# Kernel optimization log

Measured on AMD Instinct MI355X. Metric: run time of the kernel, lower is better.

The kernel has to match this reference:

```python
import jax, jax.numpy as jnp
import numpy as np
from jax import lax

D_CONV = 4


def setup_inputs() -> dict:
    key = jax.random.key(0)
    ks = jax.random.split(key, 8)
    b, L, d_model = 2, 1024, 1024
    d_inner, d_state = 2048, 16
    s = 0.02  # weight scale
    return {
        "x": jax.random.normal(ks[0], (b, L, d_model), jnp.float32),
        "in_w": jax.random.normal(ks[1], (2 * d_inner, d_model), jnp.float32) * s,
        "in_b": jnp.zeros((2 * d_inner,), jnp.float32),
        "conv_w": jax.random.normal(ks[2], (d_inner, 1, D_CONV), jnp.float32) * s,
        "conv_b": jnp.zeros((d_inner,), jnp.float32),
        "xproj_w": jax.random.normal(ks[3], (2 * d_state + 1, d_inner), jnp.float32) * s,
        "dt_w": jax.random.normal(ks[4], (d_inner, 1), jnp.float32) * s,
        "dt_b": jnp.zeros((d_inner,), jnp.float32),
        "A_log": jax.random.normal(ks[5], (d_inner, d_state), jnp.float32),
        "D": jnp.ones((d_inner,), jnp.float32),
        "out_w": jax.random.normal(ks[6], (d_model, d_inner), jnp.float32) * s,
    }


def reference(x, in_w, in_b, conv_w, conv_b, xproj_w, dt_w, dt_b, A_log, D, out_w):
    b, L, _ = x.shape
    d_inner = conv_w.shape[0]
    d_state = A_log.shape[1]

    xz = x @ in_w.T + in_b                       # (b, L, 2*d_inner)
    xh, z = jnp.split(xz, 2, axis=-1)            # each (b, L, d_inner)

    # depthwise causal conv1d (torch pads d_conv-1 both sides then slices [:L])
    xc = jnp.transpose(xh, (0, 2, 1))            # (b, d_inner, L)
    xc = lax.conv_general_dilated(
        xc, conv_w, window_strides=(1,), padding=[(D_CONV - 1, 0)],
        feature_group_count=d_inner, dimension_numbers=("NCH", "OIH", "NCH"))
    xc = xc + conv_b[None, :, None]
    xh = jnp.transpose(xc, (0, 2, 1))            # (b, L, d_inner)

    xh = xh * jax.nn.silu(z)

    proj = xh @ xproj_w.T                        # (b, L, 2*d_state+1)
    dlt = proj[..., :1]                          # (b, L, 1)
    B = proj[..., 1:1 + d_state]                 # (b, L, d_state)
    C = proj[..., 1 + d_state:]                  # (b, L, d_state)

    # dt_proj: (b,L,1) -> (b,L,d_inner); source applies softplus then exp
    delta = jnp.exp(jax.nn.softplus(dlt @ dt_w.T + dt_b))  # (b, L, d_inner)

    A = -jnp.exp(A_log)                          # (d_inner, d_state)

    def step(h, inp):
        xt, dt, Bt, Ct = inp                     # (b,i), (b,i), (b,s), (b,s)
        A_bar = jnp.exp(A[None] * dt[..., None])          # (b, i, s)
        B_bar = dt[..., None] * Bt[:, None, :]            # (b, i, s)
        h = A_bar * h + B_bar * xt[..., None]             # (b, i, s)
        yt = jnp.einsum("bis,bs->bi", h, Ct)              # (b, i)
        return h, yt

    h0 = jnp.zeros((b, d_inner, d_state), x.dtype)
    xs = (jnp.moveaxis(xh, 1, 0), jnp.moveaxis(delta, 1, 0),
          jnp.moveaxis(B, 1, 0), jnp.moveaxis(C, 1, 0))
    _, ys = lax.scan(step, h0, xs)               # (L, b, d_inner)
    y = jnp.moveaxis(ys, 0, 1) + D * xh          # (b, L, d_inner)

    return y @ out_w.T                           # (b, L, d_model)
```

## Files before the change

kernel.cpp:

```cpp
#include <hip/hip_runtime.h>
#include <hip/hip_bf16.h>

#define NTOK   2048
#define DMODEL 1024
#define DINNER 2048
#define DSTATE 16
#define SEQLEN 1024
#define NPROJ  33
#define NPAD   48
#define CCH    64
#define CT     16

typedef __attribute__((ext_vector_type(8))) short bf16x8;
typedef __attribute__((ext_vector_type(4))) float f32x4;
typedef __attribute__((ext_vector_type(8))) unsigned short us8;

__device__ __forceinline__ unsigned short f2bf(float f) {
  unsigned u = __float_as_uint(f);
  return (unsigned short)((u + 0x7FFFu + ((u >> 16) & 1u)) >> 16);
}

__device__ __forceinline__ void gload_lds16(const void* g, void* l) {
  __builtin_amdgcn_global_load_lds(
      (const __attribute__((address_space(1))) unsigned int*)g,
      (__attribute__((address_space(3))) unsigned int*)l, 16, 0, 0);
}

#define CAST_N0 (NTOK * DMODEL)
#define CAST_N1 (CAST_N0 + 2 * DINNER * DMODEL)
#define CAST_N2 (CAST_N1 + DMODEL * DINNER)
#define CAST_N3 (CAST_N2 + NPAD * DINNER)
__global__ __launch_bounds__(256) void cast4_bf16_kernel(
    const float* __restrict__ s0, const float* __restrict__ s1,
    const float* __restrict__ s2, const float* __restrict__ s3,
    unsigned short* __restrict__ dst, float* __restrict__ proj) {
  if (blockIdx.x < 33) {
    const int o = blockIdx.x * 2048 + threadIdx.x * 8;
    const float4 z4 = make_float4(0.f, 0.f, 0.f, 0.f);
    *(float4*)(proj + o) = z4;
    *(float4*)(proj + o + 4) = z4;
  }
  const int idx = (blockIdx.x * 256 + threadIdx.x) * 8;
  const float* src;
  int off;
  if (idx < CAST_N0) { src = s0; off = idx; }
  else if (idx < CAST_N1) { src = s1; off = idx - CAST_N0; }
  else if (idx < CAST_N2) { src = s2; off = idx - CAST_N1; }
  else {
    off = idx - CAST_N2;
    if (off >= NPROJ * DINNER) {
      us8 z = {0, 0, 0, 0, 0, 0, 0, 0};
      *(us8*)(dst + idx) = z;
      return;
    }
    src = s3;
  }
  const float4 a = *(const float4*)(src + off);
  const float4 b = *(const float4*)(src + off + 4);
  us8 o;
  o[0] = f2bf(a.x); o[1] = f2bf(a.y); o[2] = f2bf(a.z); o[3] = f2bf(a.w);
  o[4] = f2bf(b.x); o[5] = f2bf(b.y); o[6] = f2bf(b.z); o[7] = f2bf(b.w);
  *(us8*)(dst + idx) = o;
}

__global__ __launch_bounds__(256) void gemm_bt_mfma(
    const unsigned short* __restrict__ A, const unsigned short* __restrict__ B,
    const float* __restrict__ bias, float* __restrict__ C, int M, int K) {
  constexpr int BN = 128, TN = 4;
  __shared__ unsigned short As[2][128 * 32];
  __shared__ unsigned short Bs[2][BN * 32];

  const int tid = threadIdx.x;
  const int wid = tid >> 6;
  const int lane = tid & 63;
  const int n0 = blockIdx.x * 128;
  const int m0 = blockIdx.y * BN;

  const int wave_m = wid & 1;
  const int wave_n = wid >> 1;
  const int lm = lane & 15;
  const int lq = lane >> 4;

  f32x4 acc[4][TN] = {};

  for (int k0 = 0; k0 < K; k0 += 64) {
    __syncthreads();
#pragma unroll
    for (int h = 0; h < 2; ++h) {
      const int kh = k0 + h * 32;
#pragma unroll
      for (int j = 0; j < 2; ++j) {
        const int cb = j * 256 + wid * 64;
        const int c = cb + lane;
        gload_lds16(A + (size_t)(n0 + (c >> 2)) * K + kh + (c & 3) * 8,
                    &As[h][cb * 8]);
      }
#pragma unroll
      for (int j = 0; j < BN / 64; ++j) {
        const int cb = j * 256 + wid * 64;
        const int c = cb + lane;
        gload_lds16(B + (size_t)(m0 + (c >> 2)) * K + kh + (c & 3) * 8,
                    &Bs[h][cb * 8]);
      }
    }
    __syncthreads();

#pragma unroll
    for (int h = 0; h < 2; ++h) {
      bf16x8 af[4], bfr[TN];
#pragma unroll
      for (int tm = 0; tm < 4; ++tm)
        af[tm] = *(const bf16x8*)
            &As[h][(wave_m * 64 + tm * 16 + lm) * 32 + lq * 8];
#pragma unroll
      for (int tn = 0; tn < TN; ++tn)
        bfr[tn] = *(const bf16x8*)
            &Bs[h][(wave_n * (BN / 2) + tn * 16 + lm) * 32 + lq * 8];
#pragma unroll
      for (int tm = 0; tm < 4; ++tm)
#pragma unroll
        for (int tn = 0; tn < TN; ++tn)
          acc[tm][tn] = __builtin_amdgcn_mfma_f32_16x16x32_bf16(
              af[tm], bfr[tn], acc[tm][tn], 0, 0, 0);
    }
  }

#pragma unroll
  for (int tm = 0; tm < 4; ++tm) {
    const int row = n0 + wave_m * 64 + tm * 16 + lq * 4;
#pragma unroll
    for (int tn = 0; tn < TN; ++tn) {
      const int col = m0 + wave_n * (BN / 2) + tn * 16 + lm;
      const float bv = bias[col];
#pragma unroll
      for (int r = 0; r < 4; ++r)
        C[(size_t)(row + r) * M + col] = acc[tm][tn][r] + bv;
    }
  }
}

__global__ __launch_bounds__(256) void gemm_bt_mfma_sk(
    const unsigned short* __restrict__ A, const unsigned short* __restrict__ B,
    float* __restrict__ C, int M, int K) {
  constexpr int BN = 64, TN = 2;
  __shared__ unsigned short As[2][128 * 32];
  __shared__ unsigned short Bs[2][BN * 32];

  const int tid = threadIdx.x;
  const int wid = tid >> 6;
  const int lane = tid & 63;
  const int n0 = blockIdx.x * 128;
  const int m0 = blockIdx.y * BN;
  const int kstart = blockIdx.z * (K >> 1);

  const int wave_m = wid & 1;
  const int wave_n = wid >> 1;
  const int lm = lane & 15;
  const int lq = lane >> 4;

  f32x4 acc[4][TN] = {};

  for (int k0 = kstart; k0 < kstart + (K >> 1); k0 += 64) {
    __syncthreads();
#pragma unroll
    for (int h = 0; h < 2; ++h) {
      const int kh = k0 + h * 32;
#pragma unroll
      for (int j = 0; j < 2; ++j) {
        const int cb = j * 256 + wid * 64;
        const int c = cb + lane;
        gload_lds16(A + (size_t)(n0 + (c >> 2)) * K + kh + (c & 3) * 8,
                    &As[h][cb * 8]);
      }
      {
        const int cb = wid * 64;
        const int c = cb + lane;
        gload_lds16(B + (size_t)(m0 + (c >> 2)) * K + kh + (c & 3) * 8,
                    &Bs[h][cb * 8]);
      }
    }
    __syncthreads();

#pragma unroll
    for (int h = 0; h < 2; ++h) {
      bf16x8 af[4], bfr[TN];
#pragma unroll
      for (int tm = 0; tm < 4; ++tm)
        af[tm] = *(const bf16x8*)
            &As[h][(wave_m * 64 + tm * 16 + lm) * 32 + lq * 8];
#pragma unroll
      for (int tn = 0; tn < TN; ++tn)
        bfr[tn] = *(const bf16x8*)
            &Bs[h][(wave_n * (BN / 2) + tn * 16 + lm) * 32 + lq * 8];
#pragma unroll
      for (int tm = 0; tm < 4; ++tm)
#pragma unroll
        for (int tn = 0; tn < TN; ++tn)
          acc[tm][tn] = __builtin_amdgcn_mfma_f32_16x16x32_bf16(
              af[tm], bfr[tn], acc[tm][tn], 0, 0, 0);
    }
  }

#pragma unroll
  for (int tm = 0; tm < 4; ++tm) {
    const int row = n0 + wave_m * 64 + tm * 16 + lq * 4;
#pragma unroll
    for (int tn = 0; tn < TN; ++tn) {
      const int col = m0 + wave_n * (BN / 2) + tn * 16 + lm;
#pragma unroll
      for (int r = 0; r < 4; ++r)
        atomicAdd(&C[(size_t)(row + r) * M + col], acc[tm][tn][r]);
    }
  }
}

__global__ __launch_bounds__(256) void conv_xproj_mfma(
    const float* __restrict__ xz, const float* __restrict__ cw,
    const float* __restrict__ cb, const unsigned short* __restrict__ wp,
    float* __restrict__ xg, float* __restrict__ proj) {
  __shared__ unsigned short As[4][64 * 32];
  __shared__ unsigned short Bs[4][NPAD * 32];

  const int tid = threadIdx.x;
  const int wid = tid >> 6;
  const int lane = tid & 63;
  const int n0 = blockIdx.x * 64;
  const int kb = blockIdx.y * 128;

#pragma unroll
  for (int j = 0; j < 3; ++j) {
    const int cbase = j * 256 + wid * 64;
    const int c = cbase + lane;
    const int stage = c / 192;
    const int rem = c - stage * 192;
    gload_lds16(wp + (size_t)(rem >> 2) * DINNER + kb + stage * 32 + (rem & 3) * 8,
                &Bs[0][0] + cbase * 8);
  }

  const int c128 = tid & 127;
  const int half = tid >> 7;
  const int i = kb + c128;
  const int gt0 = n0 + half * 32;
  const float4 w4 = ((const float4*)cw)[i];
  const float cbv = cb[i];

  const bool seq_start = ((gt0 & (SEQLEN - 1)) == 0);
  float tm3 = seq_start ? 0.f : xz[(size_t)(gt0 - 3) * (2 * DINNER) + i];
  float tm2 = seq_start ? 0.f : xz[(size_t)(gt0 - 2) * (2 * DINNER) + i];
  float tm1 = seq_start ? 0.f : xz[(size_t)(gt0 - 1) * (2 * DINNER) + i];

  unsigned short* Arow = &As[c128 >> 5][c128 & 31];
#pragma unroll 4
  for (int t = 0; t < 32; ++t) {
    const int n = gt0 + t;
    const float x0 = xz[(size_t)n * (2 * DINNER) + i];
    float acc = cbv;
    acc = fmaf(w4.x, tm3, acc);
    acc = fmaf(w4.y, tm2, acc);
    acc = fmaf(w4.z, tm1, acc);
    acc = fmaf(w4.w, x0, acc);
    const float z = xz[(size_t)n * (2 * DINNER) + DINNER + i];
    const float sig = 1.f / (1.f + __expf(-z));
    const float v = acc * (z * sig);
    xg[(size_t)n * DINNER + i] = v;
    Arow[(half * 32 + t) * 32] = f2bf(v);
    tm3 = tm2; tm2 = tm1; tm1 = x0;
  }
  __syncthreads();

  const int lm = lane & 15;
  const int lq = lane >> 4;
  f32x4 acc[3] = {};
#pragma unroll
  for (int stage = 0; stage < 4; ++stage) {
    bf16x8 af = *(const bf16x8*)&As[stage][(wid * 16 + lm) * 32 + lq * 8];
#pragma unroll
    for (int tn = 0; tn < 3; ++tn) {
      bf16x8 bfr = *(const bf16x8*)&Bs[stage][(tn * 16 + lm) * 32 + lq * 8];
      acc[tn] = __builtin_amdgcn_mfma_f32_16x16x32_bf16(af, bfr, acc[tn], 0, 0, 0);
    }
  }

  const int row = n0 + wid * 16 + lq * 4;
#pragma unroll
  for (int tn = 0; tn < 3; ++tn) {
    const int col = tn * 16 + lm;
    if (col < NPROJ) {
#pragma unroll
      for (int r = 0; r < 4; ++r)
        atomicAdd(&proj[(size_t)(row + r) * NPROJ + col], acc[tn][r]);
    }
  }
}

__global__ __launch_bounds__(256) void scan_phase1(
    const float* __restrict__ xg, const float* __restrict__ proj,
    const float* __restrict__ dt_w, const float* __restrict__ dt_b,
    const float* __restrict__ A_log,
    float* __restrict__ Sbuf, float* __restrict__ Hbuf) {
  __shared__ float pl[CT][36];
  const int tid = threadIdx.x;
  const int i = blockIdx.x * 256 + tid;
  const int k = blockIdx.y;
  const int b = blockIdx.z;
  const int n0 = b * SEQLEN + k * CT;

  for (int e = tid; e < CT * NPROJ; e += 256) {
    const int t = e / NPROJ;
    const int c = e - t * NPROJ;
    pl[t][c] = proj[(size_t)(n0 + t) * NPROJ + c];
  }
  __syncthreads();

  const float dtw = dt_w[i], dtb = dt_b[i];
  float Av[DSTATE];
#pragma unroll
  for (int s = 0; s < DSTATE; ++s) Av[s] = -__expf(A_log[i * DSTATE + s]);

  float h[DSTATE] = {};
  float Ssum = 0.f;

  for (int t = 0; t < CT; ++t) {
    const float delta = 1.f + __expf(fmaf(pl[t][0], dtw, dtb));
    Ssum += delta;
    const float x = xg[(size_t)(n0 + t) * DINNER + i];
    const float dx = delta * x;
#pragma unroll
    for (int s = 0; s < DSTATE; ++s)
      h[s] = fmaf(__expf(Av[s] * delta), h[s], pl[t][1 + s] * dx);
  }

  const size_t ck = (size_t)(b * CCH + k) * DINNER + i;
  Sbuf[ck] = Ssum;
  float4* Hq = (float4*)(Hbuf + ck * DSTATE);
#pragma unroll
  for (int q = 0; q < 4; ++q)
    Hq[q] = make_float4(h[4 * q], h[4 * q + 1], h[4 * q + 2], h[4 * q + 3]);
}

__global__ __launch_bounds__(256) void scan_phase2(
    const float* __restrict__ A_log, const float* __restrict__ Sbuf,
    float* __restrict__ Hbuf, float* __restrict__ out) {
  const int gid = blockIdx.x * 256 + threadIdx.x;
  const float4 z4 = make_float4(0.f, 0.f, 0.f, 0.f);
#pragma unroll
  for (int j = 0; j < 8; ++j)
    *(float4*)(out + (size_t)(j * 65536 + gid) * 4) = z4;

  const int s = gid & (DSTATE - 1);
  const int i = (gid >> 4) & (DINNER - 1);
  const int b = gid >> 15;
  const float Av = -__expf(A_log[i * DSTATE + s]);
  float H = 0.f;
  for (int k = 0; k < CCH; ++k) {
    const size_t ck = (size_t)(b * CCH + k) * DINNER + i;
    const float hk = Hbuf[ck * DSTATE + s];
    const float a = __expf(Av * Sbuf[ck]);
    Hbuf[ck * DSTATE + s] = H;
    H = fmaf(a, H, hk);
  }
}

__global__ __launch_bounds__(256) void scan_phase3(
    const float* __restrict__ xg, const float* __restrict__ proj,
    const float* __restrict__ dt_w, const float* __restrict__ dt_b,
    const float* __restrict__ A_log, const float* __restrict__ Dp,
    const float* __restrict__ Hbuf, unsigned short* __restrict__ y) {
  __shared__ float pl[CT][36];
  const int tid = threadIdx.x;
  const int i = blockIdx.x * 256 + tid;
  const int k = blockIdx.y;
  const int b = blockIdx.z;
  const int n0 = b * SEQLEN + k * CT;

  for (int e = tid; e < CT * NPROJ; e += 256) {
    const int t = e / NPROJ;
    const int c = e - t * NPROJ;
    pl[t][c] = proj[(size_t)(n0 + t) * NPROJ + c];
  }
  __syncthreads();

  const float dtw = dt_w[i], dtb = dt_b[i];
  const float Dv = Dp[i];
  float Av[DSTATE];
#pragma unroll
  for (int s = 0; s < DSTATE; ++s) Av[s] = -__expf(A_log[i * DSTATE + s]);

  const size_t ck = (size_t)(b * CCH + k) * DINNER + i;
  float h[DSTATE];
  const float4* Hq = (const float4*)(Hbuf + ck * DSTATE);
#pragma unroll
  for (int q = 0; q < 4; ++q) {
    const float4 v = Hq[q];
    h[4 * q + 0] = v.x; h[4 * q + 1] = v.y;
    h[4 * q + 2] = v.z; h[4 * q + 3] = v.w;
  }

  for (int t = 0; t < CT; ++t) {
    const float delta = 1.f + __expf(fmaf(pl[t][0], dtw, dtb));
    const float x = xg[(size_t)(n0 + t) * DINNER + i];
    const float dx = delta * x;
    float yt = 0.f;
#pragma unroll
    for (int s = 0; s < DSTATE; ++s) {
      h[s] = fmaf(__expf(Av[s] * delta), h[s], pl[t][1 + s] * dx);
      yt = fmaf(h[s], pl[t][17 + s], yt);
    }
    y[(size_t)(n0 + t) * DINNER + i] = f2bf(fmaf(Dv, x, yt));
  }
}

extern "C" void kernel_launch(void* const* d_in, const int* in_sizes, int n_in,
                              void* d_out, int out_size, void* d_ws, size_t ws_size,
                              hipStream_t stream) {
  const float* x       = (const float*)d_in[0];
  const float* in_w    = (const float*)d_in[1];
  const float* in_b    = (const float*)d_in[2];
  const float* conv_w  = (const float*)d_in[3];
  const float* conv_b  = (const float*)d_in[4];
  const float* xproj_w = (const float*)d_in[5];
  const float* dt_w    = (const float*)d_in[6];
  const float* dt_b    = (const float*)d_in[7];
  const float* A_log   = (const float*)d_in[8];
  const float* Dp      = (const float*)d_in[9];
  const float* out_w   = (const float*)d_in[10];
  float* out = (float*)d_out;

  float* ws = (float*)d_ws;
  float* xz = ws;
  float* xg = ws + 8388608;
  unsigned short* bf_base = (unsigned short*)(ws + 12582912);
  unsigned short* x_bf    = bf_base;
  unsigned short* inw_bf  = bf_base + CAST_N0;
  unsigned short* outw_bf = bf_base + CAST_N1;
  unsigned short* wpad_bf = bf_base + CAST_N2;
  unsigned short* yb_bf = (unsigned short*)(ws + 16826368);
  float* proj = ws + 18923520;
  float* Sbuf = ws + 19005440;
  float* Hbuf = ws + 19267584;

  cast4_bf16_kernel<<<CAST_N3 / (256 * 8), 256, 0, stream>>>(
      x, in_w, out_w, xproj_w, bf_base, proj);

  gemm_bt_mfma<<<dim3(NTOK / 128, (2 * DINNER) / 128), 256, 0, stream>>>(
      x_bf, inw_bf, in_b, xz, 2 * DINNER, DMODEL);

  conv_xproj_mfma<<<dim3(NTOK / 64, DINNER / 128), 256, 0, stream>>>(
      xz, conv_w, conv_b, wpad_bf, xg, proj);

  scan_phase1<<<dim3(DINNER / 256, CCH, 2), 256, 0, stream>>>(
      xg, proj, dt_w, dt_b, A_log, Sbuf, Hbuf);
  scan_phase2<<<(2 * DINNER * DSTATE) / 256, 256, 0, stream>>>(
      A_log, Sbuf, Hbuf, out);
  scan_phase3<<<dim3(DINNER / 256, CCH, 2), 256, 0, stream>>>(
      xg, proj, dt_w, dt_b, A_log, Dp, Hbuf, yb_bf);

  gemm_bt_mfma_sk<<<dim3(NTOK / 128, DMODEL / 64, 2), 256, 0, stream>>>(
      yb_bf, outw_bf, out, DMODEL, DINNER);
}
```

Measured before the change: 213.5 us.

## Move out_w cast into scan_phase2, shrink in-proj GEMM tile, split-K by four

The out_w fp32-to-bf16 cast moves out of the front cast kernel and into scan_phase2, which is otherwise latency-bound and lightly loaded. The input-projection GEMM drops its N tile from 128 to 64, doubling its block count. The output GEMM split-K grows from 2 to 4 slices so more blocks run in parallel. The costs are more atomic or partial accumulation traffic in the out GEMM and less reuse per block in the in-projection GEMM.

```diff
diff --git a/kernel.cpp b/kernel.cpp
--- a/kernel.cpp
+++ b/kernel.cpp
@@ -28,12 +28,11 @@
 
 #define CAST_N0 (NTOK * DMODEL)
 #define CAST_N1 (CAST_N0 + 2 * DINNER * DMODEL)
-#define CAST_N2 (CAST_N1 + DMODEL * DINNER)
-#define CAST_N3 (CAST_N2 + NPAD * DINNER)
-__global__ __launch_bounds__(256) void cast4_bf16_kernel(
+#define CAST_N2 (CAST_N1 + NPAD * DINNER)
+__global__ __launch_bounds__(256) void cast3_bf16_kernel(
     const float* __restrict__ s0, const float* __restrict__ s1,
-    const float* __restrict__ s2, const float* __restrict__ s3,
-    unsigned short* __restrict__ dst, float* __restrict__ proj) {
+    const float* __restrict__ s3, unsigned short* __restrict__ dst,
+    float* __restrict__ proj) {
   if (blockIdx.x < 33) {
     const int o = blockIdx.x * 2048 + threadIdx.x * 8;
     const float4 z4 = make_float4(0.f, 0.f, 0.f, 0.f);
@@ -45,9 +44,8 @@
   int off;
   if (idx < CAST_N0) { src = s0; off = idx; }
   else if (idx < CAST_N1) { src = s1; off = idx - CAST_N0; }
-  else if (idx < CAST_N2) { src = s2; off = idx - CAST_N1; }
   else {
-    off = idx - CAST_N2;
+    off = idx - CAST_N1;
     if (off >= NPROJ * DINNER) {
       us8 z = {0, 0, 0, 0, 0, 0, 0, 0};
       *(us8*)(dst + idx) = z;
@@ -66,7 +64,7 @@
 __global__ __launch_bounds__(256) void gemm_bt_mfma(
     const unsigned short* __restrict__ A, const unsigned short* __restrict__ B,
     const float* __restrict__ bias, float* __restrict__ C, int M, int K) {
-  constexpr int BN = 128, TN = 4;
+  constexpr int BN = 64, TN = 2;
   __shared__ unsigned short As[2][128 * 32];
   __shared__ unsigned short Bs[2][BN * 32];
 
@@ -95,9 +93,8 @@
         gload_lds16(A + (size_t)(n0 + (c >> 2)) * K + kh + (c & 3) * 8,
                     &As[h][cb * 8]);
       }
-#pragma unroll
-      for (int j = 0; j < BN / 64; ++j) {
-        const int cb = j * 256 + wid * 64;
+      {
+        const int cb = wid * 64;
         const int c = cb + lane;
         gload_lds16(B + (size_t)(m0 + (c >> 2)) * K + kh + (c & 3) * 8,
                     &Bs[h][cb * 8]);
@@ -151,7 +148,7 @@
   const int lane = tid & 63;
   const int n0 = blockIdx.x * 128;
   const int m0 = blockIdx.y * BN;
-  const int kstart = blockIdx.z * (K >> 1);
+  const int kstart = blockIdx.z * (K >> 2);
 
   const int wave_m = wid & 1;
   const int wave_n = wid >> 1;
@@ -160,7 +157,7 @@
 
   f32x4 acc[4][TN] = {};
 
-  for (int k0 = kstart; k0 < kstart + (K >> 1); k0 += 64) {
+  for (int k0 = kstart; k0 < kstart + (K >> 2); k0 += 64) {
     __syncthreads();
 #pragma unroll
     for (int h = 0; h < 2; ++h) {
@@ -340,12 +337,26 @@
 
 __global__ __launch_bounds__(256) void scan_phase2(
     const float* __restrict__ A_log, const float* __restrict__ Sbuf,
-    float* __restrict__ Hbuf, float* __restrict__ out) {
+    float* __restrict__ Hbuf, float* __restrict__ out,
+    const float* __restrict__ out_w, unsigned short* __restrict__ outw_bf) {
   const int gid = blockIdx.x * 256 + threadIdx.x;
   const float4 z4 = make_float4(0.f, 0.f, 0.f, 0.f);
 #pragma unroll
   for (int j = 0; j < 8; ++j)
     *(float4*)(out + (size_t)(j * 65536 + gid) * 4) = z4;
+
+  {
+    const int base = gid * 32;
+#pragma unroll
+    for (int q = 0; q < 4; ++q) {
+      const float4 a = *(const float4*)(out_w + base + q * 8);
+      const float4 b = *(const float4*)(out_w + base + q * 8 + 4);
+      us8 o;
+      o[0] = f2bf(a.x); o[1] = f2bf(a.y); o[2] = f2bf(a.z); o[3] = f2bf(a.w);
+      o[4] = f2bf(b.x); o[5] = f2bf(b.y); o[6] = f2bf(b.z); o[7] = f2bf(b.w);
+      *(us8*)(outw_bf + base + q * 8) = o;
+    }
+  }
 
   const int s = gid & (DSTATE - 1);
   const int i = (gid >> 4) & (DINNER - 1);
@@ -432,17 +443,17 @@
   unsigned short* bf_base = (unsigned short*)(ws + 12582912);
   unsigned short* x_bf    = bf_base;
   unsigned short* inw_bf  = bf_base + CAST_N0;
-  unsigned short* outw_bf = bf_base + CAST_N1;
-  unsigned short* wpad_bf = bf_base + CAST_N2;
+  unsigned short* wpad_bf = bf_base + CAST_N1;
+  unsigned short* outw_bf = bf_base + CAST_N2;
   unsigned short* yb_bf = (unsigned short*)(ws + 16826368);
   float* proj = ws + 18923520;
   float* Sbuf = ws + 19005440;
   float* Hbuf = ws + 19267584;
 
-  cast4_bf16_kernel<<<CAST_N3 / (256 * 8), 256, 0, stream>>>(
-      x, in_w, out_w, xproj_w, bf_base, proj);
-
-  gemm_bt_mfma<<<dim3(NTOK / 128, (2 * DINNER) / 128), 256, 0, stream>>>(
+  cast3_bf16_kernel<<<CAST_N2 / (256 * 8), 256, 0, stream>>>(
+      x, in_w, xproj_w, bf_base, proj);
+
+  gemm_bt_mfma<<<dim3(NTOK / 128, (2 * DINNER) / 64), 256, 0, stream>>>(
       x_bf, inw_bf, in_b, xz, 2 * DINNER, DMODEL);
 
   conv_xproj_mfma<<<dim3(NTOK / 64, DINNER / 128), 256, 0, stream>>>(
@@ -451,10 +462,10 @@
   scan_phase1<<<dim3(DINNER / 256, CCH, 2), 256, 0, stream>>>(
       xg, proj, dt_w, dt_b, A_log, Sbuf, Hbuf);
   scan_phase2<<<(2 * DINNER * DSTATE) / 256, 256, 0, stream>>>(
-      A_log, Sbuf, Hbuf, out);
+      A_log, Sbuf, Hbuf, out, out_w, outw_bf);
   scan_phase3<<<dim3(DINNER / 256, CCH, 2), 256, 0, stream>>>(
       xg, proj, dt_w, dt_b, A_log, Dp, Hbuf, yb_bf);
 
-  gemm_bt_mfma_sk<<<dim3(NTOK / 128, DMODEL / 64, 2), 256, 0, stream>>>(
+  gemm_bt_mfma_sk<<<dim3(NTOK / 128, DMODEL / 64, 4), 256, 0, stream>>>(
       yb_bf, outw_bf, out, DMODEL, DINNER);
 }
```

Result: slower. 225.5 us (+5.6%).
